# Kernel tuning notes

Hardware: AMD Instinct MI355X
Metric: run time of the kernel (lower is better)

The kernel has to match this reference:

```python
import jax, jax.numpy as jnp
import numpy as np

N_NODES = 50000
N_EDGES = 800000
IN_DIM = 256
OUT_DIM = 128


def setup_inputs() -> dict:
    key = jax.random.key(0)
    k1, k2, k3, k4, k5 = jax.random.split(key, 5)
    adj_rows = jax.random.randint(k1, (N_EDGES,), 0, N_NODES, dtype=jnp.int32)
    adj_cols = jax.random.randint(k2, (N_EDGES,), 0, N_NODES, dtype=jnp.int32)
    adj_vals = jax.random.uniform(k3, (N_EDGES,), dtype=jnp.float32)
    x = jax.random.normal(k4, (N_NODES, IN_DIM), dtype=jnp.float32)
    # kaiming_normal-ish init for weight
    W = jax.random.normal(k5, (IN_DIM, OUT_DIM), dtype=jnp.float32) * np.sqrt(2.0 / IN_DIM)
    b = jnp.zeros((OUT_DIM,), dtype=jnp.float32)
    return {"adj_rows": adj_rows, "adj_cols": adj_cols, "adj_vals": adj_vals,
            "x": x, "W": W, "b": b}


def reference(adj_rows, adj_cols, adj_vals, x, W, b):
    # support = X @ W  (dense GEMM)
    support = x @ W  # [N, OUT_DIM]
    # sparse A @ support via edge-parallel gather + segment-sum (COO SpMM)
    msgs = adj_vals[:, None] * support[adj_cols]  # [E, OUT_DIM]
    out = jax.ops.segment_sum(msgs, adj_rows, num_segments=x.shape[0])
    return out + b
```

## Files before the change

kernel.cpp:

```cpp
#include <hip/hip_runtime.h>
#include <hip/hip_bf16.h>

#define N_NODES 50000
#define N_EDGES 800000
#define IN_DIM  256
#define OUT_DIM 128

#define NBINS        512
#define ROWS_PER_BIN 98
#define HALF_ROWS    49
#define BIN_CAP      1920
#define EPB          2048
#define NB_BIN       391
#define NB_GEMM      391
#define CUR_STRIDE   32

typedef __bf16 bf16x8 __attribute__((ext_vector_type(8)));
typedef float  f32x4  __attribute__((ext_vector_type(4)));

__device__ __forceinline__ unsigned bin_of(unsigned r) { return (r * 85599u) >> 23; }
__device__ __forceinline__ float blo(unsigned u) { return __uint_as_float(u << 16); }
__device__ __forceinline__ float bhi(unsigned u) { return __uint_as_float(u & 0xffff0000u); }

#define WF_OFF   0
#define SUP_OFF  65536
#define BIN_OFF  12865536
#define CUR_OFF  20729856

__global__ void k_prep(const float* __restrict__ W, __bf16* __restrict__ Wf,
                       int* __restrict__ bin_cursor) {
    int t = blockIdx.x * 256 + threadIdx.x;
    if (t < 32768) {
        int s = t >> 3, j = t & 7;
        int nrow = ((s >> 9) << 4) | (s & 15);
        int k    = (((s >> 4) & 3) << 3) | (((s >> 6) & 7) << 5) | j;
        Wf[t] = (__bf16)W[k * OUT_DIM + nrow];
    }
    if (t < NBINS) bin_cursor[t * CUR_STRIDE] = t * BIN_CAP;
}

__global__ __launch_bounds__(512, 4) void k_fuse(const float* __restrict__ x,
                                                 const __bf16* __restrict__ Wf,
                                                 unsigned* __restrict__ sup32,
                                                 const int* __restrict__ rows,
                                                 const int* __restrict__ cols,
                                                 const float* __restrict__ vals,
                                                 int* __restrict__ bin_cursor,
                                                 int2* __restrict__ binbuf) {
    __shared__ union {
        uint4 sB[4096];
        struct { int cur[NBINS]; int base[NBINS]; } bin;
    } sh;
    int t = threadIdx.x;

    if (blockIdx.x < NB_GEMM) {
        const uint4* wf4 = (const uint4*)Wf;
#pragma unroll
        for (int r = 0; r < 8; ++r) sh.sB[r * 512 + t] = wf4[r * 512 + t];
        __syncthreads();

        int  wave = t >> 6;
        int  lane = t & 63;
        long tile = (long)blockIdx.x * 8 + wave;
        if (tile >= 3125) return;
        int  m    = lane & 15;
        int  quad = lane >> 4;

        const float* aprow = x + (tile * 16 + m) * IN_DIM + quad * 8;

        float4 fa[16];
#pragma unroll
        for (int ks = 0; ks < 8; ++ks) {
            fa[2 * ks]     = *(const float4*)(aprow + ks * 32);
            fa[2 * ks + 1] = *(const float4*)(aprow + ks * 32 + 4);
        }
        bf16x8 ab[8];
#pragma unroll
        for (int ks = 0; ks < 8; ++ks) {
            float4 f0 = fa[2 * ks];
            float4 f1 = fa[2 * ks + 1];
            ab[ks] = (bf16x8){(__bf16)f0.x, (__bf16)f0.y, (__bf16)f0.z, (__bf16)f0.w,
                              (__bf16)f1.x, (__bf16)f1.y, (__bf16)f1.z, (__bf16)f1.w};
        }

        f32x4 acc[8];
#pragma unroll
        for (int n = 0; n < 8; ++n) acc[n] = (f32x4){0, 0, 0, 0};

        const __bf16* sbh = (const __bf16*)sh.sB;
#pragma unroll
        for (int ks = 0; ks < 8; ++ks) {
#pragma unroll
            for (int n = 0; n < 8; ++n) {
                bf16x8 bfr = *(const bf16x8*)(sbh + (((n * 8 + ks) * 64 + lane) << 3));
                acc[n] = __builtin_amdgcn_mfma_f32_16x16x32_bf16(ab[ks], bfr, acc[n], 0, 0, 0);
            }
        }

        unsigned* op = sup32 + (long)tile * 16 * 64;
#pragma unroll
        for (int r = 0; r < 4; ++r) {
#pragma unroll
            for (int n = 0; n < 4; ++n) {
                __bf16 lo = (__bf16)acc[n][r], hi = (__bf16)acc[n + 4][r];
                unsigned w = (unsigned)*(unsigned short*)&lo |
                             ((unsigned)*(unsigned short*)&hi << 16);
                op[(quad * 4 + r) * 64 + n * 16 + m] = w;
            }
        }
    } else {
        long e0 = (long)(blockIdx.x - NB_GEMM) * EPB;
        sh.bin.cur[t] = 0;
        __syncthreads();

        int2 rec[4];
        int  lrank[4];
        bool full = (e0 + EPB <= N_EDGES);

        if (full) {
#pragma unroll
            for (int k = 0; k < 4; ++k) {
                long e = e0 + k * 512 + t;
                unsigned r = (unsigned)rows[e];
                unsigned c = (unsigned)cols[e];
                float    w = vals[e];
                rec[k]   = make_int2((int)((r << 16) | c), __float_as_int(w));
                lrank[k] = atomicAdd(&sh.bin.cur[bin_of(r)], 1);
            }
        } else {
#pragma unroll
            for (int k = 0; k < 4; ++k) {
                long e = e0 + k * 512 + t;
                lrank[k] = -1;
                if (e < N_EDGES) {
                    unsigned r = (unsigned)rows[e];
                    unsigned c = (unsigned)cols[e];
                    float    w = vals[e];
                    rec[k]   = make_int2((int)((r << 16) | c), __float_as_int(w));
                    lrank[k] = atomicAdd(&sh.bin.cur[bin_of(r)], 1);
                }
            }
        }
        __syncthreads();

        sh.bin.base[t] = atomicAdd(&bin_cursor[t * CUR_STRIDE], sh.bin.cur[t]);
        __syncthreads();

        if (full) {
#pragma unroll
            for (int k = 0; k < 4; ++k) {
                unsigned bn = bin_of(((unsigned)rec[k].x) >> 16);
                int dst = sh.bin.base[bn] + lrank[k];
                if (dst < (int)(bn + 1) * BIN_CAP)
                    binbuf[dst] = rec[k];
            }
        } else {
#pragma unroll
            for (int k = 0; k < 4; ++k) {
                if (lrank[k] >= 0) {
                    unsigned bn = bin_of(((unsigned)rec[k].x) >> 16);
                    int dst = sh.bin.base[bn] + lrank[k];
                    if (dst < (int)(bn + 1) * BIN_CAP)
                        binbuf[dst] = rec[k];
                }
            }
        }
    }
}

__global__ __launch_bounds__(512, 4) void k_sg(const int* __restrict__ bin_cursor,
                                               const int2* __restrict__ binbuf,
                                               const unsigned* __restrict__ sup,
                                               const float* __restrict__ bias,
                                               float* __restrict__ out) {
    __shared__ int2 sorted_[BIN_CAP];
    __shared__ int  cnt[64], off[64], cur[64], s[64];
    int blk = blockIdx.x, t = threadIdx.x;
    int bin  = blk >> 1;
    int row0 = bin * ROWS_PER_BIN + (blk & 1) * HALF_ROWS;

    int n = bin_cursor[bin * CUR_STRIDE] - bin * BIN_CAP;
    n = n < 0 ? 0 : (n > BIN_CAP ? BIN_CAP : n);
    const int2* seg = binbuf + (long)bin * BIN_CAP;

    if (t < 64) cnt[t] = 0;
    __syncthreads();

    for (int i = t; i < n; i += 512) {
        int rl = (int)(((unsigned)seg[i].x) >> 16) - row0;
        if ((unsigned)rl < HALF_ROWS) atomicAdd(&cnt[rl], 1);
    }
    __syncthreads();

    int v = 0;
    if (t < 64) { v = cnt[t]; s[t] = v; }
    __syncthreads();
#pragma unroll
    for (int o = 1; o < 64; o <<= 1) {
        int xv = 0;
        if (t < 64 && t >= o) xv = s[t - o];
        __syncthreads();
        if (t < 64) s[t] += xv;
        __syncthreads();
    }
    if (t < 64) { off[t] = s[t] - v; cur[t] = 0; }
    __syncthreads();

    for (int i = t; i < n; i += 512) {
        int2 rec = seg[i];
        int rl = (int)(((unsigned)rec.x) >> 16) - row0;
        if ((unsigned)rl < HALF_ROWS)
            sorted_[off[rl] + atomicAdd(&cur[rl], 1)] = rec;
    }
    __syncthreads();

    int wave = t >> 6, lane = t & 63;
    float bb0 = bias[lane], bb1 = bias[64 + lane];

    for (int rl = wave; rl < HALF_ROWS; rl += 8) {
        int row = row0 + rl;
        if (row >= N_NODES) continue;
        int st = off[rl], nd = cnt[rl];
        float a0 = 0.f, a1 = 0.f;
        for (int i = 0; i < nd; i += 16) {
            int cidx[16]; unsigned u[16]; float vv[16];
#pragma unroll
            for (int j = 0; j < 16; ++j) {
                int ok = (i + j) < nd;
                int2 rec = sorted_[ok ? st + i + j : st];
                cidx[j] = rec.x & 0xffff;
                vv[j]   = ok ? __int_as_float(rec.y) : 0.f;
            }
#pragma unroll
            for (int j = 0; j < 16; ++j)
                u[j] = sup[(long)cidx[j] * 64 + lane];
#pragma unroll
            for (int j = 0; j < 16; ++j) {
                a0 += vv[j] * blo(u[j]);
                a1 += vv[j] * bhi(u[j]);
            }
        }
        out[(long)row * 128 + lane]      = a0 + bb0;
        out[(long)row * 128 + 64 + lane] = a1 + bb1;
    }
}

extern "C" void kernel_launch(void* const* d_in, const int* in_sizes, int n_in,
                              void* d_out, int out_size, void* d_ws, size_t ws_size,
                              hipStream_t stream) {
    const int*   adj_rows = (const int*)  d_in[0];
    const int*   adj_cols = (const int*)  d_in[1];
    const float* adj_vals = (const float*)d_in[2];
    const float* x        = (const float*)d_in[3];
    const float* W        = (const float*)d_in[4];
    const float* b        = (const float*)d_in[5];
    float* out = (float*)d_out;

    char* ws = (char*)d_ws;
    __bf16*   Wf         = (__bf16*)  (ws + WF_OFF);
    unsigned* sup32      = (unsigned*)(ws + SUP_OFF);
    int2*     binbuf     = (int2*)    (ws + BIN_OFF);
    int*      bin_cursor = (int*)     (ws + CUR_OFF);

    k_prep<<<128, 256, 0, stream>>>(W, Wf, bin_cursor);
    k_fuse<<<NB_GEMM + NB_BIN, 512, 0, stream>>>(x, Wf, sup32,
                                                 adj_rows, adj_cols, adj_vals,
                                                 bin_cursor, binbuf);
    k_sg  <<<NBINS * 2, 512, 0, stream>>>(bin_cursor, binbuf, sup32, b, out);
}
```

Before: 151.2 us.

## Fuse prep, bin/GEMM and segment-gather into one cooperative persistent kernel

Replaces the three kernel launches with one cooperative kernel of 512 blocks that uses grid-wide syncs between the weight-prep, binning+GEMM and gather phases. Blocks 0-390 bin edges and blocks from 121 up run GEMM tiles, so the two jobs overlap inside the same blocks. In the last phase each block handles one bin's two half-row groups sequentially. This removes launch gaps and kernel boundaries at the cost of grid sync overhead, less parallelism in the gather phase (512 blocks instead of 1024) and serialised work in the overlapping blocks. The old three-kernel path is kept as a fallback if the cooperative launch fails.

Result: slower. 575.7 us (+280.7%).

```diff
diff --git a/kernel.cpp b/kernel.cpp
--- a/kernel.cpp
+++ b/kernel.cpp
@@ -1,5 +1,8 @@
 #include <hip/hip_runtime.h>
 #include <hip/hip_bf16.h>
+#include <hip/hip_cooperative_groups.h>
+
+namespace cg = cooperative_groups;
 
 #define N_NODES 50000
 #define N_EDGES 800000
@@ -14,6 +17,8 @@
 #define NB_BIN       391
 #define NB_GEMM      391
 #define CUR_STRIDE   32
+#define GRID         512
+#define GEMM_B0      121
 
 typedef __bf16 bf16x8 __attribute__((ext_vector_type(8)));
 typedef float  f32x4  __attribute__((ext_vector_type(4)));
@@ -146,23 +151,13 @@
         sh.bin.base[t] = atomicAdd(&bin_cursor[t * CUR_STRIDE], sh.bin.cur[t]);
         __syncthreads();
 
-        if (full) {
-#pragma unroll
-            for (int k = 0; k < 4; ++k) {
+#pragma unroll
+        for (int k = 0; k < 4; ++k) {
+            if (lrank[k] >= 0) {
                 unsigned bn = bin_of(((unsigned)rec[k].x) >> 16);
                 int dst = sh.bin.base[bn] + lrank[k];
                 if (dst < (int)(bn + 1) * BIN_CAP)
                     binbuf[dst] = rec[k];
-            }
-        } else {
-#pragma unroll
-            for (int k = 0; k < 4; ++k) {
-                if (lrank[k] >= 0) {
-                    unsigned bn = bin_of(((unsigned)rec[k].x) >> 16);
-                    int dst = sh.bin.base[bn] + lrank[k];
-                    if (dst < (int)(bn + 1) * BIN_CAP)
-                        binbuf[dst] = rec[k];
-                }
             }
         }
     }
@@ -245,6 +240,222 @@
     }
 }
 
+__global__ __launch_bounds__(512, 4) void k_all(
+    const float* __restrict__ W, const float* __restrict__ x,
+    const int* __restrict__ rows, const int* __restrict__ cols,
+    const float* __restrict__ vals, const float* __restrict__ bias,
+    float* __restrict__ out, __bf16* __restrict__ Wf,
+    unsigned* __restrict__ sup32, int2* __restrict__ binbuf,
+    int* __restrict__ bin_cursor) {
+    __shared__ union {
+        uint4 sB[4096];
+        struct { int cur[NBINS]; int base[NBINS]; } bin;
+        struct { int2 sorted_[BIN_CAP];
+                 int cnt[64], off[64], cur[64], s[64]; } sg;
+    } sh;
+    int t   = threadIdx.x;
+    int bid = blockIdx.x;
+
+    {
+        int g = bid * 512 + t;
+        if (g < 32768) {
+            int s = g >> 3, j = g & 7;
+            int nrow = ((s >> 9) << 4) | (s & 15);
+            int k    = (((s >> 4) & 3) << 3) | (((s >> 6) & 7) << 5) | j;
+            Wf[g] = (__bf16)W[k * OUT_DIM + nrow];
+        }
+        int c = g - 32768;
+        if ((unsigned)c < NBINS) bin_cursor[c * CUR_STRIDE] = c * BIN_CAP;
+    }
+    __threadfence_system();
+    cg::this_grid().sync();
+    __threadfence_system();
+
+    if (bid < NB_BIN) {
+        long e0 = (long)bid * EPB;
+        sh.bin.cur[t] = 0;
+        __syncthreads();
+
+        int2 rec[4];
+        int  lrank[4];
+        bool full = (e0 + EPB <= N_EDGES);
+
+        if (full) {
+#pragma unroll
+            for (int k = 0; k < 4; ++k) {
+                long e = e0 + k * 512 + t;
+                unsigned r = (unsigned)rows[e];
+                unsigned c = (unsigned)cols[e];
+                float    w = vals[e];
+                rec[k]   = make_int2((int)((r << 16) | c), __float_as_int(w));
+                lrank[k] = atomicAdd(&sh.bin.cur[bin_of(r)], 1);
+            }
+        } else {
+#pragma unroll
+            for (int k = 0; k < 4; ++k) {
+                long e = e0 + k * 512 + t;
+                lrank[k] = -1;
+                if (e < N_EDGES) {
+                    unsigned r = (unsigned)rows[e];
+                    unsigned c = (unsigned)cols[e];
+                    float    w = vals[e];
+                    rec[k]   = make_int2((int)((r << 16) | c), __float_as_int(w));
+                    lrank[k] = atomicAdd(&sh.bin.cur[bin_of(r)], 1);
+                }
+            }
+        }
+        __syncthreads();
+
+        sh.bin.base[t] = atomicAdd(&bin_cursor[t * CUR_STRIDE], sh.bin.cur[t]);
+        __syncthreads();
+
+#pragma unroll
+        for (int k = 0; k < 4; ++k) {
+            if (lrank[k] >= 0) {
+                unsigned bn = bin_of(((unsigned)rec[k].x) >> 16);
+                int dst = sh.bin.base[bn] + lrank[k];
+                if (dst < (int)(bn + 1) * BIN_CAP)
+                    binbuf[dst] = rec[k];
+            }
+        }
+    }
+    __syncthreads();
+
+    if (bid >= GEMM_B0) {
+        const uint4* wf4 = (const uint4*)Wf;
+#pragma unroll
+        for (int r = 0; r < 8; ++r) sh.sB[r * 512 + t] = wf4[r * 512 + t];
+        __syncthreads();
+
+        int  wave = t >> 6;
+        int  lane = t & 63;
+        long tile = (long)(bid - GEMM_B0) * 8 + wave;
+        if (tile < 3125) {
+            int m    = lane & 15;
+            int quad = lane >> 4;
+
+            const float* aprow = x + (tile * 16 + m) * IN_DIM + quad * 8;
+
+            float4 fa[16];
+#pragma unroll
+            for (int ks = 0; ks < 8; ++ks) {
+                fa[2 * ks]     = *(const float4*)(aprow + ks * 32);
+                fa[2 * ks + 1] = *(const float4*)(aprow + ks * 32 + 4);
+            }
+            bf16x8 ab[8];
+#pragma unroll
+            for (int ks = 0; ks < 8; ++ks) {
+                float4 f0 = fa[2 * ks];
+                float4 f1 = fa[2 * ks + 1];
+                ab[ks] = (bf16x8){(__bf16)f0.x, (__bf16)f0.y, (__bf16)f0.z, (__bf16)f0.w,
+                                  (__bf16)f1.x, (__bf16)f1.y, (__bf16)f1.z, (__bf16)f1.w};
+            }
+
+            f32x4 acc[8];
+#pragma unroll
+            for (int n = 0; n < 8; ++n) acc[n] = (f32x4){0, 0, 0, 0};
+
+            const __bf16* sbh = (const __bf16*)sh.sB;
+#pragma unroll
+            for (int ks = 0; ks < 8; ++ks) {
+#pragma unroll
+                for (int n = 0; n < 8; ++n) {
+                    bf16x8 bfr = *(const bf16x8*)(sbh + (((n * 8 + ks) * 64 + lane) << 3));
+                    acc[n] = __builtin_amdgcn_mfma_f32_16x16x32_bf16(ab[ks], bfr, acc[n], 0, 0, 0);
+                }
+            }
+
+            unsigned* op = sup32 + (long)tile * 16 * 64;
+#pragma unroll
+            for (int r = 0; r < 4; ++r) {
+#pragma unroll
+                for (int n = 0; n < 4; ++n) {
+                    __bf16 lo = (__bf16)acc[n][r], hi = (__bf16)acc[n + 4][r];
+                    unsigned w = (unsigned)*(unsigned short*)&lo |
+                                 ((unsigned)*(unsigned short*)&hi << 16);
+                    op[(quad * 4 + r) * 64 + n * 16 + m] = w;
+                }
+            }
+        }
+    }
+    __threadfence_system();
+    cg::this_grid().sync();
+    __threadfence_system();
+
+    {
+        int wave = t >> 6, lane = t & 63;
+        float bb0 = bias[lane], bb1 = bias[64 + lane];
+
+        int bin = bid;
+        int n = bin_cursor[bin * CUR_STRIDE] - bin * BIN_CAP;
+        n = n < 0 ? 0 : (n > BIN_CAP ? BIN_CAP : n);
+        const int2* seg = binbuf + (long)bin * BIN_CAP;
+
+        for (int u = 0; u < 2; ++u) {
+            int row0 = bin * ROWS_PER_BIN + u * HALF_ROWS;
+
+            if (t < 64) sh.sg.cnt[t] = 0;
+            __syncthreads();
+
+            for (int i = t; i < n; i += 512) {
+                int rl = (int)(((unsigned)seg[i].x) >> 16) - row0;
+                if ((unsigned)rl < HALF_ROWS) atomicAdd(&sh.sg.cnt[rl], 1);
+            }
+            __syncthreads();
+
+            int v = 0;
+            if (t < 64) { v = sh.sg.cnt[t]; sh.sg.s[t] = v; }
+            __syncthreads();
+#pragma unroll
+            for (int o = 1; o < 64; o <<= 1) {
+                int xv = 0;
+                if (t < 64 && t >= o) xv = sh.sg.s[t - o];
+                __syncthreads();
+                if (t < 64) sh.sg.s[t] += xv;
+                __syncthreads();
+            }
+            if (t < 64) { sh.sg.off[t] = sh.sg.s[t] - v; sh.sg.cur[t] = 0; }
+            __syncthreads();
+
+            for (int i = t; i < n; i += 512) {
+                int2 rec = seg[i];
+                int rl = (int)(((unsigned)rec.x) >> 16) - row0;
+                if ((unsigned)rl < HALF_ROWS)
+                    sh.sg.sorted_[sh.sg.off[rl] + atomicAdd(&sh.sg.cur[rl], 1)] = rec;
+            }
+            __syncthreads();
+
+            for (int rl = wave; rl < HALF_ROWS; rl += 8) {
+                int row = row0 + rl;
+                if (row >= N_NODES) continue;
+                int st = sh.sg.off[rl], nd = sh.sg.cnt[rl];
+                float a0 = 0.f, a1 = 0.f;
+                for (int i = 0; i < nd; i += 16) {
+                    int cidx[16]; unsigned uu[16]; float vv[16];
+#pragma unroll
+                    for (int j = 0; j < 16; ++j) {
+                        int ok = (i + j) < nd;
+                        int2 rec = sh.sg.sorted_[ok ? st + i + j : st];
+                        cidx[j] = rec.x & 0xffff;
+                        vv[j]   = ok ? __int_as_float(rec.y) : 0.f;
+                    }
+#pragma unroll
+                    for (int j = 0; j < 16; ++j)
+                        uu[j] = sup32[(long)cidx[j] * 64 + lane];
+#pragma unroll
+                    for (int j = 0; j < 16; ++j) {
+                        a0 += vv[j] * blo(uu[j]);
+                        a1 += vv[j] * bhi(uu[j]);
+                    }
+                }
+                out[(long)row * 128 + lane]      = a0 + bb0;
+                out[(long)row * 128 + 64 + lane] = a1 + bb1;
+            }
+            __syncthreads();
+        }
+    }
+}
+
 extern "C" void kernel_launch(void* const* d_in, const int* in_sizes, int n_in,
                               void* d_out, int out_size, void* d_ws, size_t ws_size,
                               hipStream_t stream) {
@@ -262,9 +473,21 @@
     int2*     binbuf     = (int2*)    (ws + BIN_OFF);
     int*      bin_cursor = (int*)     (ws + CUR_OFF);
 
-    k_prep<<<128, 256, 0, stream>>>(W, Wf, bin_cursor);
-    k_fuse<<<NB_GEMM + NB_BIN, 512, 0, stream>>>(x, Wf, sup32,
-                                                 adj_rows, adj_cols, adj_vals,
-                                                 bin_cursor, binbuf);
-    k_sg  <<<NBINS * 2, 512, 0, stream>>>(bin_cursor, binbuf, sup32, b, out);
+    const float* W_a = W; const float* x_a = x;
+    const int* rows_a = adj_rows; const int* cols_a = adj_cols;
+    const float* vals_a = adj_vals; const float* b_a = b;
+    void* args[] = {
+        (void*)&W_a, (void*)&x_a, (void*)&rows_a, (void*)&cols_a,
+        (void*)&vals_a, (void*)&b_a, (void*)&out, (void*)&Wf,
+        (void*)&sup32, (void*)&binbuf, (void*)&bin_cursor
+    };
+    hipError_t err = hipLaunchCooperativeKernel((const void*)k_all, dim3(GRID),
+                                                dim3(512), args, 0, stream);
+    if (err != hipSuccess) {
+        k_prep<<<128, 256, 0, stream>>>(W, Wf, bin_cursor);
+        k_fuse<<<NB_GEMM + NB_BIN, 512, 0, stream>>>(x, Wf, sup32,
+                                                     adj_rows, adj_cols, adj_vals,
+                                                     bin_cursor, binbuf);
+        k_sg  <<<NBINS * 2, 512, 0, stream>>>(bin_cursor, binbuf, sup32, b, out);
+    }
 }
```
